# Performance work log

Hardware: AMD Instinct MI355X
Metric: run time of the kernel (lower is better)

Reference implementation:

```python
import jax, jax.numpy as jnp
import numpy as np

N_NODES = 100000


def setup_inputs() -> dict:
    key = jax.random.key(0)
    k1, k2, k3, k4, k5 = jax.random.split(key, 5)
    x = jax.random.normal(k1, (N_NODES, 128), dtype=jnp.float32)
    edge_index = jax.random.randint(k2, (2, 1600000), 0, N_NODES, dtype=jnp.int64)
    # Linear weights stored torch-style: W is [out_features, in_features]
    W_l = jax.random.normal(k3, (128, 128), dtype=jnp.float32) * 0.05
    b_l = jax.random.normal(k4, (128,), dtype=jnp.float32) * 0.05
    W_r = jax.random.normal(k5, (128, 128), dtype=jnp.float32) * 0.05
    return {"x": x, "edge_index": edge_index, "W_l": W_l, "b_l": b_l, "W_r": W_r}


def reference(x, edge_index, W_l, b_l, W_r):
    # x_l = lin_l(x)  -> [N, out]
    x_l = x @ W_l.T + b_l
    src, dst = edge_index[0], edge_index[1]
    # sparse adjacency matmul: mean aggregation of neighbor features into each dst node
    agg = jax.ops.segment_sum(x_l[src], dst, num_segments=N_NODES)  # [N, out]
    deg = jax.ops.segment_sum(jnp.ones_like(src, dtype=x.dtype), dst, num_segments=N_NODES)
    y = agg / jnp.maximum(deg, 1.0)[:, None]
    # root/self transform (no bias) and elementwise add
    out_r = x @ W_r.T
    return y + out_r
```

## Files before the change

### kernel.cpp

```cpp
#include <hip/hip_runtime.h>
#include <hip/hip_bf16.h>

#define N_NODES 100000
#define N_EDGES 1600000
#define FEAT 128
#define NBINS 2048
#define BIN_NODES 49
#define PBLK 250
#define CHUNK (N_EDGES / PBLK)
#define NTBL (NBINS + 1)
#define CSR_MAX 1280
#define PREP_BLOCKS (N_NODES * FEAT / 8 / 512)
#define WCONV_BLOCKS 8

typedef __bf16 bf16x8 __attribute__((ext_vector_type(8)));
typedef unsigned short ushort8 __attribute__((ext_vector_type(8)));
typedef float f32x4 __attribute__((ext_vector_type(4)));
typedef float f32x2 __attribute__((ext_vector_type(2)));

__device__ __forceinline__ unsigned short f2bf_bits(float f) {
    unsigned u = __builtin_bit_cast(unsigned, f);
    unsigned r = (u + 0x7fffu + ((u >> 16) & 1u)) >> 16;
    return (unsigned short)r;
}

__device__ __forceinline__ ushort8 cvt8(float4 a, float4 b) {
    ushort8 u;
    u[0] = f2bf_bits(a.x); u[1] = f2bf_bits(a.y);
    u[2] = f2bf_bits(a.z); u[3] = f2bf_bits(a.w);
    u[4] = f2bf_bits(b.x); u[5] = f2bf_bits(b.y);
    u[6] = f2bf_bits(b.z); u[7] = f2bf_bits(b.w);
    return u;
}

__global__ __launch_bounds__(512) void preppart_kernel(
    const float* __restrict__ x, unsigned short* __restrict__ xbf,
    unsigned int* __restrict__ x8, const int* __restrict__ ei,
    int* __restrict__ offtbl, int* __restrict__ ebin,
    const float* __restrict__ Wl, const float* __restrict__ Wr,
    unsigned short* __restrict__ wlbf, unsigned short* __restrict__ wrbf) {
    __shared__ int h[NBINS];
    __shared__ int wsum[8];
    const int tid = threadIdx.x;

    if (blockIdx.x >= PBLK + PREP_BLOCKS) {
        int t = (blockIdx.x - PBLK - PREP_BLOCKS) * 512 + tid;
        const float* src;
        unsigned short* dst;
        int off;
        if (t < 2048) { src = Wl; dst = wlbf; off = t * 8; }
        else          { src = Wr; dst = wrbf; off = (t - 2048) * 8; }
        float4 a = *(const float4*)(src + off);
        float4 b = *(const float4*)(src + off + 4);
        *(ushort8*)(dst + off) = cvt8(a, b);
        return;
    }

    if (blockIdx.x >= PBLK) {
        int t = (blockIdx.x - PBLK) * 512 + tid;
        float4 a = ((const float4*)x)[t * 2];
        float4 b = ((const float4*)x)[t * 2 + 1];
        ((ushort8*)xbf)[t] = cvt8(a, b);
        int w0 = __builtin_amdgcn_cvt_pk_fp8_f32(a.x, a.y, 0, false);
        w0     = __builtin_amdgcn_cvt_pk_fp8_f32(a.z, a.w, w0, true);
        int w1 = __builtin_amdgcn_cvt_pk_fp8_f32(b.x, b.y, 0, false);
        w1     = __builtin_amdgcn_cvt_pk_fp8_f32(b.z, b.w, w1, true);
        uint2 p; p.x = (unsigned)w0; p.y = (unsigned)w1;
        ((uint2*)x8)[t] = p;
        return;
    }

    const int b = blockIdx.x;
    const int lane = tid & 63, wid = tid >> 6;

    for (int i = tid; i < NBINS; i += 512) h[i] = 0;
    __syncthreads();

    const int4* dsts = (const int4*)(ei + N_EDGES + b * CHUNK);
    for (int i = tid; i < CHUNK / 4; i += 512) {
        int4 d = dsts[i];
        atomicAdd(&h[d.x / BIN_NODES], 1);
        atomicAdd(&h[d.y / BIN_NODES], 1);
        atomicAdd(&h[d.z / BIN_NODES], 1);
        atomicAdd(&h[d.w / BIN_NODES], 1);
    }
    __syncthreads();

    const int i0 = tid * 4;
    int v0 = h[i0], v1 = h[i0 + 1], v2 = h[i0 + 2], v3 = h[i0 + 3];
    const int s = v0 + v1 + v2 + v3;
    int incl = s;
    #pragma unroll
    for (int d = 1; d < 64; d <<= 1) {
        int up = __shfl_up(incl, d);
        if (lane >= d) incl += up;
    }
    if (lane == 63) wsum[wid] = incl;
    __syncthreads();
    if (tid == 0) {
        int run = 0;
        #pragma unroll
        for (int i = 0; i < 8; ++i) { int v = wsum[i]; wsum[i] = run; run += v; }
    }
    __syncthreads();
    int run = wsum[wid] + incl - s + b * CHUNK;
    int* otb = offtbl + (size_t)b * NTBL;
    h[i0] = run; otb[i0] = run; run += v0;
    h[i0 + 1] = run; otb[i0 + 1] = run; run += v1;
    h[i0 + 2] = run; otb[i0 + 2] = run; run += v2;
    h[i0 + 3] = run; otb[i0 + 3] = run; run += v3;
    if (tid == 0) otb[NBINS] = (b + 1) * CHUNK;
    __syncthreads();

    const int4* srcs = (const int4*)(ei + b * CHUNK);
    for (int i = tid; i < CHUNK / 4; i += 512) {
        int4 s4 = srcs[i];
        int4 d4 = dsts[i];
        int bin, ln, pos;
        bin = d4.x / BIN_NODES; ln = d4.x - bin * BIN_NODES;
        pos = atomicAdd(&h[bin], 1); ebin[pos] = s4.x | (ln << 17);
        bin = d4.y / BIN_NODES; ln = d4.y - bin * BIN_NODES;
        pos = atomicAdd(&h[bin], 1); ebin[pos] = s4.y | (ln << 17);
        bin = d4.z / BIN_NODES; ln = d4.z - bin * BIN_NODES;
        pos = atomicAdd(&h[bin], 1); ebin[pos] = s4.z | (ln << 17);
        bin = d4.w / BIN_NODES; ln = d4.w - bin * BIN_NODES;
        pos = atomicAdd(&h[bin], 1); ebin[pos] = s4.w | (ln << 17);
    }
}

#define ACC8(v)                                                             \
    {                                                                       \
        acc2[0] += __builtin_amdgcn_cvt_pk_f32_fp8((int)(v).x, false);      \
        acc2[1] += __builtin_amdgcn_cvt_pk_f32_fp8((int)(v).x, true);       \
        acc2[2] += __builtin_amdgcn_cvt_pk_f32_fp8((int)(v).y, false);      \
        acc2[3] += __builtin_amdgcn_cvt_pk_f32_fp8((int)(v).y, true);       \
    }

__global__ __launch_bounds__(256) void agg_kernel(
    const unsigned char* __restrict__ x8, const int* __restrict__ offtbl,
    const int* __restrict__ ebin, unsigned short* __restrict__ xbarbf,
    int* __restrict__ degs) {
    __shared__ int lcnt[BIN_NODES];
    __shared__ int loff[BIN_NODES];
    __shared__ int lcur[BIN_NODES];
    __shared__ int lraw[CSR_MAX];
    __shared__ int lcsr[CSR_MAX];
    __shared__ int wtot[4];

    const int bid = blockIdx.x, tid = threadIdx.x;
    const int b = (bid & 7) * (NBINS / 8) + (bid >> 3);
    int nb = N_NODES - b * BIN_NODES;
    if (nb <= 0) return;
    if (nb > BIN_NODES) nb = BIN_NODES;

    const int lane = tid & 63, wave = tid >> 6;

    int st = 0, L = 0;
    if (tid < PBLK) {
        st = offtbl[(size_t)tid * NTBL + b];
        L  = offtbl[(size_t)tid * NTBL + b + 1] - st;
    }
    if (tid < BIN_NODES) lcnt[tid] = 0;

    int incl = L;
    #pragma unroll
    for (int d = 1; d < 64; d <<= 1) {
        int up = __shfl_up(incl, d);
        if (lane >= d) incl += up;
    }
    if (lane == 63) wtot[wave] = incl;
    __syncthreads();
    int woff = 0;
    #pragma unroll
    for (int w = 0; w < 4; ++w) woff += (w < wave) ? wtot[w] : 0;
    const int pfx = woff + incl - L;

    for (int i = 0; i < L; ++i) {
        int v = ebin[st + i];
        lraw[pfx + i] = v;
        atomicAdd(&lcnt[v >> 17], 1);
    }
    __syncthreads();

    if (wave == 0) {
        int c = (lane < BIN_NODES) ? lcnt[lane] : 0;
        int ic = c;
        #pragma unroll
        for (int d = 1; d < 64; d <<= 1) {
            int up = __shfl_up(ic, d);
            if (lane >= d) ic += up;
        }
        if (lane < BIN_NODES) {
            loff[lane] = ic - c;
            lcur[lane] = ic - c;
        }
    }
    __syncthreads();

    for (int i = 0; i < L; ++i) {
        int v = lraw[pfx + i];
        int pos = atomicAdd(&lcur[v >> 17], 1);
        lcsr[pos] = v & 0x1FFFF;
    }
    __syncthreads();

    const int g = lane >> 4;
    const unsigned c8 = (lane & 15) * 8;
    for (int ln = wave; ln < nb; ln += 4) {
        const int deg = lcnt[ln];
        const int off = loff[ln];
        f32x2 acc2[4];
        #pragma unroll
        for (int i = 0; i < 4; ++i) acc2[i] = (f32x2){0.f, 0.f};
        for (int base = 0; base < deg; base += 32) {
            int j0 = base + g;
            bool p0 = j0 < deg,       p1 = j0 + 4 < deg,  p2 = j0 + 8 < deg;
            bool p3 = j0 + 12 < deg,  p4 = j0 + 16 < deg, p5 = j0 + 20 < deg;
            bool p6 = j0 + 24 < deg,  p7 = j0 + 28 < deg;
            unsigned sA = (unsigned)(p0 ? lcsr[off + j0]      : lcsr[off]);
            unsigned sB = (unsigned)(p1 ? lcsr[off + j0 + 4]  : lcsr[off]);
            unsigned sC = (unsigned)(p2 ? lcsr[off + j0 + 8]  : lcsr[off]);
            unsigned sD = (unsigned)(p3 ? lcsr[off + j0 + 12] : lcsr[off]);
            unsigned sE = (unsigned)(p4 ? lcsr[off + j0 + 16] : lcsr[off]);
            unsigned sF = (unsigned)(p5 ? lcsr[off + j0 + 20] : lcsr[off]);
            unsigned sG = (unsigned)(p6 ? lcsr[off + j0 + 24] : lcsr[off]);
            unsigned sH = (unsigned)(p7 ? lcsr[off + j0 + 28] : lcsr[off]);
            uint2 va = *(const uint2*)(x8 + ((sA << 7) + c8));
            uint2 vb = *(const uint2*)(x8 + ((sB << 7) + c8));
            uint2 vc = *(const uint2*)(x8 + ((sC << 7) + c8));
            uint2 vd = *(const uint2*)(x8 + ((sD << 7) + c8));
            uint2 ve = *(const uint2*)(x8 + ((sE << 7) + c8));
            uint2 vf = *(const uint2*)(x8 + ((sF << 7) + c8));
            uint2 vg = *(const uint2*)(x8 + ((sG << 7) + c8));
            uint2 vh = *(const uint2*)(x8 + ((sH << 7) + c8));
            if (p0) ACC8(va);
            if (p1) ACC8(vb);
            if (p2) ACC8(vc);
            if (p3) ACC8(vd);
            if (p4) ACC8(ve);
            if (p5) ACC8(vf);
            if (p6) ACC8(vg);
            if (p7) ACC8(vh);
        }
        #pragma unroll
        for (int i = 0; i < 4; ++i) {
            #pragma unroll
            for (int k = 0; k < 2; ++k) {
                acc2[i][k] += __shfl_xor(acc2[i][k], 16);
                acc2[i][k] += __shfl_xor(acc2[i][k], 32);
            }
        }
        const int n = b * BIN_NODES + ln;
        if (lane < 16) {
            float inv = 1.0f / (float)(deg > 0 ? deg : 1);
            ushort8 o;
            #pragma unroll
            for (int i = 0; i < 4; ++i) {
                o[2 * i]     = f2bf_bits(acc2[i][0] * inv);
                o[2 * i + 1] = f2bf_bits(acc2[i][1] * inv);
            }
            *(ushort8*)(xbarbf + (size_t)n * FEAT + c8) = o;
        }
        if (lane == 0) degs[n] = deg;
    }
}

__global__ __launch_bounds__(256) void gemm_kernel(
    const unsigned short* __restrict__ xbf, const unsigned short* __restrict__ xbarbf,
    const unsigned short* __restrict__ wlbf, const float* __restrict__ bl,
    const unsigned short* __restrict__ wrbf, const int* __restrict__ degs,
    float* __restrict__ out) {

    __shared__ unsigned short lM[32][136];
    __shared__ unsigned short lX[32][136];

    const int tid = threadIdx.x;
    const int wave = tid >> 6, lane = tid & 63;
    const int l15 = lane & 15, lhi = lane >> 4;
    const int colbase = wave * 32;

    bf16x8 bB[2][8];
    float biasv[2];
    #pragma unroll
    for (int ct = 0; ct < 2; ++ct) {
        int col = colbase + ct * 16 + l15;
        biasv[ct] = bl[col];
        #pragma unroll
        for (int s = 0; s < 4; ++s) {
            int kb = lhi * 8 + s * 32;
            bB[ct][s]     = __builtin_bit_cast(bf16x8, *(const ushort8*)(wlbf + col * 128 + kb));
            bB[ct][4 + s] = __builtin_bit_cast(bf16x8, *(const ushort8*)(wrbf + col * 128 + kb));
        }
    }

    const int xcd = blockIdx.x & 7;
    const int sub = blockIdx.x >> 3;
    const int tile0 = xcd * 390 + (xcd < 5 ? xcd : 5);
    const int cnt = (xcd < 5) ? 391 : 390;
    for (int t = sub; t < cnt; t += 128) {
        const int tile = tile0 + t;
        const int row0 = tile * 32;
        {
            int r = tid >> 3;
            int c0 = (tid & 7) * 16;
            const unsigned short* sm = xbarbf + (size_t)(row0 + r) * FEAT + c0;
            const unsigned short* sx = xbf + (size_t)(row0 + r) * FEAT + c0;
            *(ushort8*)&lM[r][c0]     = *(const ushort8*)(sm);
            *(ushort8*)&lM[r][c0 + 8] = *(const ushort8*)(sm + 8);
            *(ushort8*)&lX[r][c0]     = *(const ushort8*)(sx);
            *(ushort8*)&lX[r][c0 + 8] = *(const ushort8*)(sx + 8);
        }
        __syncthreads();

        f32x4 acc[2][2];
        #pragma unroll
        for (int rh = 0; rh < 2; ++rh)
            #pragma unroll
            for (int ct = 0; ct < 2; ++ct) acc[rh][ct] = (f32x4){0.f, 0.f, 0.f, 0.f};

        #pragma unroll
        for (int rh = 0; rh < 2; ++rh) {
            int arow = rh * 16 + l15;
            bf16x8 aM[4], aX[4];
            #pragma unroll
            for (int s = 0; s < 4; ++s) {
                aM[s] = __builtin_bit_cast(bf16x8, *(const ushort8*)&lM[arow][lhi * 8 + s * 32]);
                aX[s] = __builtin_bit_cast(bf16x8, *(const ushort8*)&lX[arow][lhi * 8 + s * 32]);
            }
            #pragma unroll
            for (int ct = 0; ct < 2; ++ct) {
                f32x4 a = acc[rh][ct];
                #pragma unroll
                for (int s = 0; s < 4; ++s)
                    a = __builtin_amdgcn_mfma_f32_16x16x32_bf16(aM[s], bB[ct][s], a, 0, 0, 0);
                #pragma unroll
                for (int s = 0; s < 4; ++s)
                    a = __builtin_amdgcn_mfma_f32_16x16x32_bf16(aX[s], bB[ct][4 + s], a, 0, 0, 0);
                acc[rh][ct] = a;
            }
        }

        #pragma unroll
        for (int rh = 0; rh < 2; ++rh)
            #pragma unroll
            for (int ct = 0; ct < 2; ++ct) {
                int col = colbase + ct * 16 + l15;
                #pragma unroll
                for (int j = 0; j < 4; ++j) {
                    int r = row0 + rh * 16 + lhi * 4 + j;
                    float bias = (degs[r] > 0) ? biasv[ct] : 0.f;
                    out[(size_t)r * FEAT + col] = acc[rh][ct][j] + bias;
                }
            }
        __syncthreads();
    }
}

extern "C" void kernel_launch(void* const* d_in, const int* in_sizes, int n_in,
                              void* d_out, int out_size, void* d_ws, size_t ws_size,
                              hipStream_t stream) {
    const float* x  = (const float*)d_in[0];
    const int*   ei = (const int*)d_in[1];
    const float* Wl = (const float*)d_in[2];
    const float* bl = (const float*)d_in[3];
    const float* Wr = (const float*)d_in[4];
    float* out = (float*)d_out;

    unsigned short* xbf    = (unsigned short*)d_ws;
    unsigned short* xbarbf = xbf + (size_t)N_NODES * FEAT;
    unsigned int* x8       = (unsigned int*)(xbarbf + (size_t)N_NODES * FEAT);
    int* degs   = (int*)(x8 + (size_t)N_NODES * FEAT / 4);
    int* offtbl = degs + N_NODES;
    unsigned short* wlbf = (unsigned short*)(offtbl + (size_t)PBLK * NTBL);
    unsigned short* wrbf = wlbf + 16384;
    int* ebin   = (int*)(wrbf + 16384);

    preppart_kernel<<<PBLK + PREP_BLOCKS + WCONV_BLOCKS, 512, 0, stream>>>(
        x, xbf, x8, ei, offtbl, ebin, Wl, Wr, wlbf, wrbf);
    agg_kernel<<<NBINS, 256, 0, stream>>>((const unsigned char*)x8, offtbl, ebin, xbarbf, degs);
    gemm_kernel<<<1024, 256, 0, stream>>>(xbf, xbarbf, wlbf, bl, wrbf, degs, out);
}
```

Measured before the change: 91.15 us.

## Fuse neighbor aggregation and dense GEMM into a single per-bin kernel

Merges the aggregation and GEMM kernels. Each bin block keeps its mean-aggregated bf16 rows in shared memory and runs both MFMA products (mean·W_l and x·W_r) on its 49-node tile before writing the output directly. This removes the global round trip of the xbar and degree arrays and one kernel launch. The gather inner loop is also shortened from 8 to 4 outstanding loads per step, which may lower memory-level parallelism. Extra shared memory and accumulator registers may reduce occupancy, and MFMA tiles padded to 64 rows for 49 real nodes waste some compute.

```diff
diff --git a/kernel.cpp b/kernel.cpp
--- a/kernel.cpp
+++ b/kernel.cpp
@@ -136,16 +136,18 @@
         acc2[3] += __builtin_amdgcn_cvt_pk_f32_fp8((int)(v).y, true);       \
     }
 
-__global__ __launch_bounds__(256) void agg_kernel(
-    const unsigned char* __restrict__ x8, const int* __restrict__ offtbl,
-    const int* __restrict__ ebin, unsigned short* __restrict__ xbarbf,
-    int* __restrict__ degs) {
+__global__ __launch_bounds__(256) void aggemm_kernel(
+    const unsigned char* __restrict__ x8, const unsigned short* __restrict__ xbf,
+    const int* __restrict__ offtbl, const int* __restrict__ ebin,
+    const unsigned short* __restrict__ wlbf, const unsigned short* __restrict__ wrbf,
+    const float* __restrict__ bl, float* __restrict__ out) {
     __shared__ int lcnt[BIN_NODES];
     __shared__ int loff[BIN_NODES];
     __shared__ int lcur[BIN_NODES];
     __shared__ int lraw[CSR_MAX];
     __shared__ int lcsr[CSR_MAX];
     __shared__ int wtot[4];
+    __shared__ unsigned short lA[64][136];
 
     const int bid = blockIdx.x, tid = threadIdx.x;
     const int b = (bid & 7) * (NBINS / 8) + (bid >> 3);
@@ -212,35 +214,21 @@
         f32x2 acc2[4];
         #pragma unroll
         for (int i = 0; i < 4; ++i) acc2[i] = (f32x2){0.f, 0.f};
-        for (int base = 0; base < deg; base += 32) {
-            int j0 = base + g;
-            bool p0 = j0 < deg,       p1 = j0 + 4 < deg,  p2 = j0 + 8 < deg;
-            bool p3 = j0 + 12 < deg,  p4 = j0 + 16 < deg, p5 = j0 + 20 < deg;
-            bool p6 = j0 + 24 < deg,  p7 = j0 + 28 < deg;
-            unsigned sA = (unsigned)(p0 ? lcsr[off + j0]      : lcsr[off]);
-            unsigned sB = (unsigned)(p1 ? lcsr[off + j0 + 4]  : lcsr[off]);
-            unsigned sC = (unsigned)(p2 ? lcsr[off + j0 + 8]  : lcsr[off]);
-            unsigned sD = (unsigned)(p3 ? lcsr[off + j0 + 12] : lcsr[off]);
-            unsigned sE = (unsigned)(p4 ? lcsr[off + j0 + 16] : lcsr[off]);
-            unsigned sF = (unsigned)(p5 ? lcsr[off + j0 + 20] : lcsr[off]);
-            unsigned sG = (unsigned)(p6 ? lcsr[off + j0 + 24] : lcsr[off]);
-            unsigned sH = (unsigned)(p7 ? lcsr[off + j0 + 28] : lcsr[off]);
+        for (int base = 0; base < deg; base += 16) {
+            int j0 = base + g, j1 = j0 + 4, j2 = j0 + 8, j3 = j0 + 12;
+            bool pA = j0 < deg, pB = j1 < deg, pC = j2 < deg, pD = j3 < deg;
+            unsigned sA = (unsigned)(pA ? lcsr[off + j0] : lcsr[off]);
+            unsigned sB = (unsigned)(pB ? lcsr[off + j1] : lcsr[off]);
+            unsigned sC = (unsigned)(pC ? lcsr[off + j2] : lcsr[off]);
+            unsigned sD = (unsigned)(pD ? lcsr[off + j3] : lcsr[off]);
             uint2 va = *(const uint2*)(x8 + ((sA << 7) + c8));
             uint2 vb = *(const uint2*)(x8 + ((sB << 7) + c8));
             uint2 vc = *(const uint2*)(x8 + ((sC << 7) + c8));
             uint2 vd = *(const uint2*)(x8 + ((sD << 7) + c8));
-            uint2 ve = *(const uint2*)(x8 + ((sE << 7) + c8));
-            uint2 vf = *(const uint2*)(x8 + ((sF << 7) + c8));
-            uint2 vg = *(const uint2*)(x8 + ((sG << 7) + c8));
-            uint2 vh = *(const uint2*)(x8 + ((sH << 7) + c8));
-            if (p0) ACC8(va);
-            if (p1) ACC8(vb);
-            if (p2) ACC8(vc);
-            if (p3) ACC8(vd);
-            if (p4) ACC8(ve);
-            if (p5) ACC8(vf);
-            if (p6) ACC8(vg);
-            if (p7) ACC8(vh);
+            if (pA) ACC8(va);
+            if (pB) ACC8(vb);
+            if (pC) ACC8(vc);
+            if (pD) ACC8(vd);
         }
         #pragma unroll
         for (int i = 0; i < 4; ++i) {
@@ -250,7 +238,6 @@
                 acc2[i][k] += __shfl_xor(acc2[i][k], 32);
             }
         }
-        const int n = b * BIN_NODES + ln;
         if (lane < 16) {
             float inv = 1.0f / (float)(deg > 0 ? deg : 1);
             ushort8 o;
@@ -259,101 +246,104 @@
                 o[2 * i]     = f2bf_bits(acc2[i][0] * inv);
                 o[2 * i + 1] = f2bf_bits(acc2[i][1] * inv);
             }
-            *(ushort8*)(xbarbf + (size_t)n * FEAT + c8) = o;
-        }
-        if (lane == 0) degs[n] = deg;
-    }
-}
-
-__global__ __launch_bounds__(256) void gemm_kernel(
-    const unsigned short* __restrict__ xbf, const unsigned short* __restrict__ xbarbf,
-    const unsigned short* __restrict__ wlbf, const float* __restrict__ bl,
-    const unsigned short* __restrict__ wrbf, const int* __restrict__ degs,
-    float* __restrict__ out) {
-
-    __shared__ unsigned short lM[32][136];
-    __shared__ unsigned short lX[32][136];
-
-    const int tid = threadIdx.x;
-    const int wave = tid >> 6, lane = tid & 63;
+            *(ushort8*)&lA[ln][c8] = o;
+        }
+    }
+    __syncthreads();
+
     const int l15 = lane & 15, lhi = lane >> 4;
     const int colbase = wave * 32;
-
-    bf16x8 bB[2][8];
+    f32x4 acc[4][2];
+    #pragma unroll
+    for (int rh = 0; rh < 4; ++rh)
+        #pragma unroll
+        for (int ct = 0; ct < 2; ++ct) acc[rh][ct] = (f32x4){0.f, 0.f, 0.f, 0.f};
+
     float biasv[2];
-    #pragma unroll
-    for (int ct = 0; ct < 2; ++ct) {
-        int col = colbase + ct * 16 + l15;
-        biasv[ct] = bl[col];
-        #pragma unroll
-        for (int s = 0; s < 4; ++s) {
-            int kb = lhi * 8 + s * 32;
-            bB[ct][s]     = __builtin_bit_cast(bf16x8, *(const ushort8*)(wlbf + col * 128 + kb));
-            bB[ct][4 + s] = __builtin_bit_cast(bf16x8, *(const ushort8*)(wrbf + col * 128 + kb));
-        }
-    }
-
-    const int xcd = blockIdx.x & 7;
-    const int sub = blockIdx.x >> 3;
-    const int tile0 = xcd * 390 + (xcd < 5 ? xcd : 5);
-    const int cnt = (xcd < 5) ? 391 : 390;
-    for (int t = sub; t < cnt; t += 128) {
-        const int tile = tile0 + t;
-        const int row0 = tile * 32;
-        {
-            int r = tid >> 3;
-            int c0 = (tid & 7) * 16;
-            const unsigned short* sm = xbarbf + (size_t)(row0 + r) * FEAT + c0;
-            const unsigned short* sx = xbf + (size_t)(row0 + r) * FEAT + c0;
-            *(ushort8*)&lM[r][c0]     = *(const ushort8*)(sm);
-            *(ushort8*)&lM[r][c0 + 8] = *(const ushort8*)(sm + 8);
-            *(ushort8*)&lX[r][c0]     = *(const ushort8*)(sx);
-            *(ushort8*)&lX[r][c0 + 8] = *(const ushort8*)(sx + 8);
-        }
-        __syncthreads();
-
-        f32x4 acc[2][2];
-        #pragma unroll
-        for (int rh = 0; rh < 2; ++rh)
-            #pragma unroll
-            for (int ct = 0; ct < 2; ++ct) acc[rh][ct] = (f32x4){0.f, 0.f, 0.f, 0.f};
-
-        #pragma unroll
-        for (int rh = 0; rh < 2; ++rh) {
+    {
+        bf16x8 bW[2][4];
+        #pragma unroll
+        for (int ct = 0; ct < 2; ++ct) {
+            int col = colbase + ct * 16 + l15;
+            biasv[ct] = bl[col];
+            #pragma unroll
+            for (int s = 0; s < 4; ++s)
+                bW[ct][s] = __builtin_bit_cast(bf16x8, *(const ushort8*)(wlbf + col * 128 + lhi * 8 + s * 32));
+        }
+        #pragma unroll
+        for (int rh = 0; rh < 4; ++rh) {
             int arow = rh * 16 + l15;
-            bf16x8 aM[4], aX[4];
-            #pragma unroll
-            for (int s = 0; s < 4; ++s) {
-                aM[s] = __builtin_bit_cast(bf16x8, *(const ushort8*)&lM[arow][lhi * 8 + s * 32]);
-                aX[s] = __builtin_bit_cast(bf16x8, *(const ushort8*)&lX[arow][lhi * 8 + s * 32]);
-            }
+            bf16x8 aF[4];
+            #pragma unroll
+            for (int s = 0; s < 4; ++s)
+                aF[s] = __builtin_bit_cast(bf16x8, *(const ushort8*)&lA[arow][lhi * 8 + s * 32]);
             #pragma unroll
             for (int ct = 0; ct < 2; ++ct) {
                 f32x4 a = acc[rh][ct];
                 #pragma unroll
                 for (int s = 0; s < 4; ++s)
-                    a = __builtin_amdgcn_mfma_f32_16x16x32_bf16(aM[s], bB[ct][s], a, 0, 0, 0);
+                    a = __builtin_amdgcn_mfma_f32_16x16x32_bf16(aF[s], bW[ct][s], a, 0, 0, 0);
+                acc[rh][ct] = a;
+            }
+        }
+    }
+    __syncthreads();
+
+    {
+        int r = tid >> 2;
+        int cq = (tid & 3) * 32;
+        int n = b * BIN_NODES + r;
+        if (n > N_NODES - 1) n = N_NODES - 1;
+        const unsigned short* src = xbf + (size_t)n * FEAT + cq;
+        *(ushort8*)&lA[r][cq]      = *(const ushort8*)(src);
+        *(ushort8*)&lA[r][cq + 8]  = *(const ushort8*)(src + 8);
+        *(ushort8*)&lA[r][cq + 16] = *(const ushort8*)(src + 16);
+        *(ushort8*)&lA[r][cq + 24] = *(const ushort8*)(src + 24);
+    }
+    __syncthreads();
+
+    {
+        bf16x8 bW[2][4];
+        #pragma unroll
+        for (int ct = 0; ct < 2; ++ct) {
+            int col = colbase + ct * 16 + l15;
+            #pragma unroll
+            for (int s = 0; s < 4; ++s)
+                bW[ct][s] = __builtin_bit_cast(bf16x8, *(const ushort8*)(wrbf + col * 128 + lhi * 8 + s * 32));
+        }
+        #pragma unroll
+        for (int rh = 0; rh < 4; ++rh) {
+            int arow = rh * 16 + l15;
+            bf16x8 aF[4];
+            #pragma unroll
+            for (int s = 0; s < 4; ++s)
+                aF[s] = __builtin_bit_cast(bf16x8, *(const ushort8*)&lA[arow][lhi * 8 + s * 32]);
+            #pragma unroll
+            for (int ct = 0; ct < 2; ++ct) {
+                f32x4 a = acc[rh][ct];
                 #pragma unroll
                 for (int s = 0; s < 4; ++s)
-                    a = __builtin_amdgcn_mfma_f32_16x16x32_bf16(aX[s], bB[ct][4 + s], a, 0, 0, 0);
+                    a = __builtin_amdgcn_mfma_f32_16x16x32_bf16(aF[s], bW[ct][s], a, 0, 0, 0);
                 acc[rh][ct] = a;
             }
         }
-
-        #pragma unroll
-        for (int rh = 0; rh < 2; ++rh)
-            #pragma unroll
-            for (int ct = 0; ct < 2; ++ct) {
-                int col = colbase + ct * 16 + l15;
-                #pragma unroll
-                for (int j = 0; j < 4; ++j) {
-                    int r = row0 + rh * 16 + lhi * 4 + j;
-                    float bias = (degs[r] > 0) ? biasv[ct] : 0.f;
-                    out[(size_t)r * FEAT + col] = acc[rh][ct][j] + bias;
+    }
+
+    #pragma unroll
+    for (int rh = 0; rh < 4; ++rh)
+        #pragma unroll
+        for (int ct = 0; ct < 2; ++ct) {
+            int col = colbase + ct * 16 + l15;
+            #pragma unroll
+            for (int j = 0; j < 4; ++j) {
+                int rl = rh * 16 + lhi * 4 + j;
+                if (rl < nb) {
+                    int n = b * BIN_NODES + rl;
+                    float bias = (lcnt[rl] > 0) ? biasv[ct] : 0.f;
+                    out[(size_t)n * FEAT + col] = acc[rh][ct][j] + bias;
                 }
             }
-        __syncthreads();
-    }
+        }
 }
 
 extern "C" void kernel_launch(void* const* d_in, const int* in_sizes, int n_in,
@@ -366,17 +356,15 @@
     const float* Wr = (const float*)d_in[4];
     float* out = (float*)d_out;
 
-    unsigned short* xbf    = (unsigned short*)d_ws;
-    unsigned short* xbarbf = xbf + (size_t)N_NODES * FEAT;
-    unsigned int* x8       = (unsigned int*)(xbarbf + (size_t)N_NODES * FEAT);
-    int* degs   = (int*)(x8 + (size_t)N_NODES * FEAT / 4);
-    int* offtbl = degs + N_NODES;
+    unsigned short* xbf = (unsigned short*)d_ws;
+    unsigned int* x8    = (unsigned int*)(xbf + (size_t)N_NODES * FEAT);
+    int* offtbl = (int*)(x8 + (size_t)N_NODES * FEAT / 4);
     unsigned short* wlbf = (unsigned short*)(offtbl + (size_t)PBLK * NTBL);
     unsigned short* wrbf = wlbf + 16384;
     int* ebin   = (int*)(wrbf + 16384);
 
     preppart_kernel<<<PBLK + PREP_BLOCKS + WCONV_BLOCKS, 512, 0, stream>>>(
         x, xbf, x8, ei, offtbl, ebin, Wl, Wr, wlbf, wrbf);
-    agg_kernel<<<NBINS, 256, 0, stream>>>((const unsigned char*)x8, offtbl, ebin, xbarbf, degs);
-    gemm_kernel<<<1024, 256, 0, stream>>>(xbf, xbarbf, wlbf, bl, wrbf, degs, out);
-}
+    aggemm_kernel<<<NBINS, 256, 0, stream>>>((const unsigned char*)x8, xbf,
+                                             offtbl, ebin, wlbf, wrbf, bl, out);
+}
```

Result: slower. 96.35 us (+5.7%).
